# Optimization experiments

Measured on AMD Instinct MI355X. Metric: run time of the kernel, lower is better.

Reference implementation:

```python
import jax, jax.numpy as jnp
import numpy as np

B, S, VOCAB, D_MODEL, N_KERNELS, KSIZE, N_CLASSES = 8, 2048, 32000, 512, 256, 9, 4096
PAD = KSIZE // 2  # source uses kernel_size/2 (py2 int div)


def setup_inputs() -> dict:
    key = jax.random.key(0)
    ks = jax.random.split(key, 7)
    return {
        "text": jax.random.randint(ks[0], (B, S), 0, VOCAB),
        "embed_table": jax.random.normal(ks[1], (VOCAB, D_MODEL), dtype=jnp.float32) * 0.02,
        "conv_w": jax.random.normal(ks[2], (N_KERNELS, D_MODEL, KSIZE), dtype=jnp.float32) * 0.02,
        "conv_b": jax.random.normal(ks[3], (N_KERNELS,), dtype=jnp.float32) * 0.02,
        "U_w": jax.random.normal(ks[4], (N_CLASSES, N_KERNELS), dtype=jnp.float32) * 0.02,
        "final_w": jax.random.normal(ks[5], (N_CLASSES, N_KERNELS), dtype=jnp.float32) * 0.02,
        "final_b": jax.random.normal(ks[6], (N_CLASSES,), dtype=jnp.float32) * 0.02,
    }


def reference(text, embed_table, conv_w, conv_b, U_w, final_w, final_b):
    # Embedding lookup (tgt_embed); dropout is identity in eval mode.
    x = embed_table[text]                                  # [B, S, D]
    # Conv1d over sequence: NCH layout, OIH kernel, same-length padding.
    xc = jax.lax.conv_general_dilated(
        x.transpose(0, 2, 1), conv_w,
        window_strides=(1,), padding=[(PAD, PAD)],
        dimension_numbers=("NCH", "OIH", "NCH"))
    x = jnp.tanh(xc.transpose(0, 2, 1) + conv_b)           # [B, S, K]
    # Shared-query label attention: scores [B, n_classes, S].
    scores = jnp.einsum("ck,bsk->bcs", U_w, x)
    alpha = jax.nn.softmax(scores, axis=2)
    m = jnp.einsum("bcs,bsk->bck", alpha, x)               # [B, C, K]
    y = jnp.sum(final_w * m, axis=2) + final_b             # [B, C]
    return y
```

## Files before the change

### kernel.cpp

```cpp
#include <hip/hip_runtime.h>
#include <math.h>

#define B 8
#define S 2048
#define D_MODEL 512
#define NK 256
#define KSZ 9
#define NC 4096
#define PADW 4
#define SSPLIT 4
#define CM 64
#define CW (CM + 8)
#define NSTG (KSZ * 16)
#define NTILES ((S / SSPLIT) / 32)

typedef __attribute__((ext_vector_type(8))) short bf16x8;
typedef __attribute__((ext_vector_type(4))) float f32x4;

static __device__ __forceinline__ unsigned short f2bf(float f) {
    unsigned int u = __float_as_uint(f);
    unsigned int r = (u + 0x7fffu + ((u >> 16) & 1u)) >> 16;
    return (unsigned short)r;
}

#define GLOAD_LDS16(g, l) __builtin_amdgcn_global_load_lds( \
    (const __attribute__((address_space(1))) void*)(g),     \
    (__attribute__((address_space(3))) void*)(l), 16, 0, 0)

#define PREP_W (KSZ * NK * D_MODEL)
#define PREP_UF (NC * NK)
#define PREP_N (PREP_W + (2 * PREP_UF) / 4)
__global__ __launch_bounds__(256) void prep_all(
    const float* __restrict__ w, unsigned short* __restrict__ wtb,
    const float* __restrict__ U, unsigned short* __restrict__ Ub,
    const float* __restrict__ F, unsigned short* __restrict__ Fb)
{
    const float LOG2E = 1.44269504088896340736f;
    int idx = blockIdx.x * 256 + threadIdx.x;
    if (idx < PREP_W) {
        int dd  = idx & 31;
        int k   = (idx >> 5) & (NK - 1);
        int stg = idx >> 13;
        int t = stg >> 4, h = stg & 15;
        wtb[idx] = f2bf(w[((size_t)k * D_MODEL + h * 32 + dd) * KSZ + t]);
        return;
    }
    idx -= PREP_W;
    if (idx < PREP_UF / 4) {
        float4 v = ((const float4*)U)[idx];
        ushort4 o;
        o.x = f2bf(v.x * LOG2E); o.y = f2bf(v.y * LOG2E);
        o.z = f2bf(v.z * LOG2E); o.w = f2bf(v.w * LOG2E);
        ((ushort4*)Ub)[idx] = o;
        return;
    }
    idx -= PREP_UF / 4;
    if (idx < PREP_UF / 4) {
        float4 v = ((const float4*)F)[idx];
        ushort4 o;
        o.x = f2bf(v.x); o.y = f2bf(v.y);
        o.z = f2bf(v.z); o.w = f2bf(v.w);
        ((ushort4*)Fb)[idx] = o;
    }
}

__global__ __launch_bounds__(512, 2) void conv_mfma(
    const int* __restrict__ text, const float* __restrict__ emb,
    const unsigned short* __restrict__ wtb, const float* __restrict__ bias,
    unsigned short* __restrict__ xf)
{
    __shared__ unsigned short xs[CW * D_MODEL];
    const int b  = blockIdx.x >> 5;
    const int s0 = (blockIdx.x & 31) * CM;
    const int tid = threadIdx.x;

    for (int u = tid; u < CW * 64; u += 512) {
        int row = u >> 6, c = u & 63;
        int gs = s0 + row - PADW;
        float4 v0 = make_float4(0.f, 0.f, 0.f, 0.f), v1 = v0;
        if (gs >= 0 && gs < S) {
            int tok = text[b * S + gs];
            const float4* e4 = (const float4*)(emb + (size_t)tok * D_MODEL + c * 8);
            v0 = e4[0]; v1 = e4[1];
        }
        union { bf16x8 v; unsigned short us[8]; } pk;
        pk.us[0] = f2bf(v0.x); pk.us[1] = f2bf(v0.y);
        pk.us[2] = f2bf(v0.z); pk.us[3] = f2bf(v0.w);
        pk.us[4] = f2bf(v1.x); pk.us[5] = f2bf(v1.y);
        pk.us[6] = f2bf(v1.z); pk.us[7] = f2bf(v1.w);
        int phys = c ^ (row & 7);
        *(bf16x8*)(xs + row * D_MODEL + phys * 8) = pk.v;
    }
    __syncthreads();

    const int wv   = tid >> 6;
    const int lane = tid & 63;
    const int cl   = lane & 15;
    const int quad = lane >> 4;
    const int n0   = wv * 32;

    bf16x8 A0[4], A1[4], A2[4], B0[2], B1[2], B2[2];
    f32x4 acc[4][2] = {};

    #define LDB(BB, stg)                                                      \
        {                                                                     \
            const unsigned short* wp = wtb + (size_t)(stg) * (NK * 32)        \
                                       + (n0 + cl) * 32 + quad * 8;           \
            BB[0] = *(const bf16x8*)(wp);                                     \
            BB[1] = *(const bf16x8*)(wp + 16 * 32);                           \
        }
    #define LDA(AA, stg)                                                      \
        {                                                                     \
            int t_ = (stg) >> 4, h_ = (stg) & 15;                             \
            _Pragma("unroll")                                                 \
            for (int ms = 0; ms < 4; ms++) {                                  \
                int row = cl + ms * 16 + t_;                                  \
                int ph  = (h_ * 4 + quad) ^ (row & 7);                        \
                AA[ms] = *(const bf16x8*)(xs + row * D_MODEL + ph * 8);       \
            }                                                                 \
        }
    #define FENCE asm volatile("" ::: "memory");
    #define DOMFMA(AA, BB)                                                    \
        _Pragma("unroll")                                                     \
        for (int ms = 0; ms < 4; ms++) {                                      \
            acc[ms][0] = __builtin_amdgcn_mfma_f32_16x16x32_bf16(AA[ms], BB[0], acc[ms][0], 0, 0, 0); \
            acc[ms][1] = __builtin_amdgcn_mfma_f32_16x16x32_bf16(AA[ms], BB[1], acc[ms][1], 0, 0, 0); \
        }

    LDB(B0, 0) LDA(A0, 0) LDB(B1, 1) LDA(A1, 1) LDB(B2, 2) LDA(A2, 2) FENCE

    for (int ss = 0; ss < NSTG; ss += 3) {
        DOMFMA(A0, B0)
        if (ss + 3 < NSTG) { LDB(B0, ss + 3) LDA(A0, ss + 3) FENCE }
        DOMFMA(A1, B1)
        if (ss + 4 < NSTG) { LDB(B1, ss + 4) LDA(A1, ss + 4) FENCE }
        DOMFMA(A2, B2)
        if (ss + 5 < NSTG) { LDB(B2, ss + 5) LDA(A2, ss + 5) FENCE }
    }

    #pragma unroll
    for (int ns = 0; ns < 2; ns++) {
        const int k = n0 + ns * 16 + cl;
        const float bk = bias[k];
        #pragma unroll
        for (int ms = 0; ms < 4; ms++) {
            #pragma unroll
            for (int r = 0; r < 4; r++) {
                int s = s0 + ms * 16 + quad * 4 + r;
                float v = acc[ms][ns][r] + bk;
                float e = __expf(2.f * v);
                float th = 1.f - 2.f / (e + 1.f);
                xf[((size_t)b * S + s) * NK + k] = f2bf(th);
            }
        }
    }
}

#define WAITVM4 asm volatile("s_waitcnt vmcnt(4)" ::: "memory")
#define WAITVM0 asm volatile("s_waitcnt vmcnt(0)" ::: "memory")
__global__ __launch_bounds__(256, 3) void attn_mfma(
    const unsigned short* __restrict__ xf, const unsigned short* __restrict__ Ub,
    const unsigned short* __restrict__ Fb, float* __restrict__ pl,
    float* __restrict__ pg)
{
    __shared__ unsigned short xsa[3 * 32 * NK];
    const int b    = blockIdx.z;
    const int sp   = blockIdx.y;
    const int tid  = threadIdx.x;
    const int wv   = tid >> 6;
    const int lane = tid & 63;
    const int cl   = lane & 15;
    const int quad = lane >> 4;
    const int c0   = blockIdx.x * 64 + wv * 16;
    const int wvu  = __builtin_amdgcn_readfirstlane(wv);

    bf16x8 uf[8], ff[8];
    {
        const unsigned short* up = Ub + (size_t)(c0 + cl) * NK + quad * 8;
        const unsigned short* fp = Fb + (size_t)(c0 + cl) * NK + quad * 8;
        #pragma unroll
        for (int kk = 0; kk < 8; kk++) {
            uf[kk] = *(const bf16x8*)(up + kk * 32);
            ff[kk] = *(const bf16x8*)(fp + kk * 32);
        }
    }

    const int sbeg = sp * (S / SSPLIT);
    const unsigned short* xb = xf + ((size_t)b * S + sbeg) * NK;

    const unsigned short* ssrc[4];
    unsigned short* sdst[4];
    #pragma unroll
    for (int j = 0; j < 4; j++) {
        int C = j * 256 + tid;
        int r = C >> 5, p = C & 31;
        int jl = p ^ (r & 7);
        ssrc[j] = xb + (size_t)r * NK + jl * 8;
        sdst[j] = xsa + j * 2048 + wvu * 512;
    }

    #define STAGE(bb, t)                                                      \
        {                                                                     \
            _Pragma("unroll")                                                 \
            for (int j = 0; j < 4; j++)                                       \
                GLOAD_LDS16(ssrc[j] + (t) * (32 * NK), sdst[j] + (bb) * 8192);\
        }

    STAGE(0, 0)
    STAGE(1, 1)

    const int swz = cl & 7;
    const unsigned short* pE = xsa + cl * NK + (quad ^ swz) * 8;
    const unsigned short* pO = xsa + cl * NK + ((quad + 4) ^ swz) * 8;

    float l = 0.f, G = 0.f;

    #pragma unroll
    for (int t = 0; t < NTILES; t++) {
        if (t + 1 < NTILES) { WAITVM4; } else { WAITVM0; }
        __builtin_amdgcn_s_barrier();
        if (t + 2 < NTILES) STAGE((t + 2) % 3, t + 2)

        const int buf = t % 3;
        f32x4 sa[2] = {}, ga[2] = {};
        #pragma unroll
        for (int kk = 0; kk < 8; kk++) {
            const unsigned short* pp = (kk & 1) ? pO : pE;
            const int eo = buf * 8192 + (kk >> 1) * 64;
            bf16x8 a0 = *(const bf16x8*)(pp + eo);
            bf16x8 a1 = *(const bf16x8*)(pp + eo + 16 * NK);
            sa[0] = __builtin_amdgcn_mfma_f32_16x16x32_bf16(a0, uf[kk], sa[0], 0, 0, 0);
            ga[0] = __builtin_amdgcn_mfma_f32_16x16x32_bf16(a0, ff[kk], ga[0], 0, 0, 0);
            sa[1] = __builtin_amdgcn_mfma_f32_16x16x32_bf16(a1, uf[kk], sa[1], 0, 0, 0);
            ga[1] = __builtin_amdgcn_mfma_f32_16x16x32_bf16(a1, ff[kk], ga[1], 0, 0, 0);
        }

        #pragma unroll
        for (int r = 0; r < 4; r++) {
            float e0 = __builtin_amdgcn_exp2f(sa[0][r]);
            float e1 = __builtin_amdgcn_exp2f(sa[1][r]);
            l += e0 + e1;
            G += e0 * ga[0][r] + e1 * ga[1][r];
        }
    }

    l += __shfl_xor(l, 16); l += __shfl_xor(l, 32);
    G += __shfl_xor(G, 16); G += __shfl_xor(G, 32);
    if (lane < 16) {
        size_t idx = ((size_t)b * SSPLIT + sp) * NC + c0 + lane;
        pl[idx] = l; pg[idx] = G;
    }
}

__global__ __launch_bounds__(256) void combine_kernel(
    const float* __restrict__ pl, const float* __restrict__ pg,
    const float* __restrict__ fb, float* __restrict__ out)
{
    int idx = blockIdx.x * 256 + threadIdx.x;
    if (idx >= B * NC) return;
    int b = idx / NC, c = idx % NC;
    float l = 0.f, g = 0.f;
    #pragma unroll
    for (int sp = 0; sp < SSPLIT; sp++) {
        size_t i = ((size_t)b * SSPLIT + sp) * NC + c;
        l += pl[i];
        g += pg[i];
    }
    out[idx] = g / l + fb[c];
}

extern "C" void kernel_launch(void* const* d_in, const int* in_sizes, int n_in,
                              void* d_out, int out_size, void* d_ws, size_t ws_size,
                              hipStream_t stream) {
    const int*   text   = (const int*)  d_in[0];
    const float* emb    = (const float*)d_in[1];
    const float* conv_w = (const float*)d_in[2];
    const float* conv_b = (const float*)d_in[3];
    const float* U_w    = (const float*)d_in[4];
    const float* F_w    = (const float*)d_in[5];
    const float* f_b    = (const float*)d_in[6];
    float* out = (float*)d_out;

    char* ws = (char*)d_ws;
    unsigned short* xf  = (unsigned short*)ws; ws += (size_t)B * S * NK * 2;
    unsigned short* wtb = (unsigned short*)ws; ws += (size_t)KSZ * NK * D_MODEL * 2;
    unsigned short* Ub  = (unsigned short*)ws; ws += (size_t)NC * NK * 2;
    unsigned short* Fb  = (unsigned short*)ws; ws += (size_t)NC * NK * 2;
    float* pl = (float*)ws; ws += (size_t)SSPLIT * B * NC * 4;
    float* pg = (float*)ws; ws += (size_t)SSPLIT * B * NC * 4;

    prep_all<<<dim3((PREP_N + 255) / 256), 256, 0, stream>>>(conv_w, wtb, U_w, Ub, F_w, Fb);
    conv_mfma<<<dim3(B * S / CM), 512, 0, stream>>>(text, emb, wtb, conv_b, xf);
    attn_mfma<<<dim3(NC / 64, SSPLIT, B), 256, 0, stream>>>(xf, Ub, Fb, pl, pg);
    combine_kernel<<<dim3((B * NC + 255) / 256), 256, 0, stream>>>(pl, pg, f_b, out);
}
```

Measured before the change: 214.1 us.

## Switch attention kernel to 32x32x16 MFMA with 128 classes per block

Each wave in the attention kernel now covers 32 classes instead of 16 and uses 32x32x16 bf16 MFMA in place of pairs of 16x16x32 MFMAs. Grid blocks each handle 128 classes, which halves the number of blocks and the reloads of the x tiles from global memory and LDS per class. The cost is twice as many U/F fragment registers held per wave, and launch bounds drop from 3 to 2 blocks per CU, which reduces occupancy. The LDS swizzle addressing is recomputed to match the new fragment layout.

```diff
diff --git a/kernel.cpp b/kernel.cpp
--- a/kernel.cpp
+++ b/kernel.cpp
@@ -16,6 +16,7 @@
 
 typedef __attribute__((ext_vector_type(8))) short bf16x8;
 typedef __attribute__((ext_vector_type(4))) float f32x4;
+typedef __attribute__((ext_vector_type(16))) float f32x16;
 
 static __device__ __forceinline__ unsigned short f2bf(float f) {
     unsigned int u = __float_as_uint(f);
@@ -158,7 +159,7 @@
 
 #define WAITVM4 asm volatile("s_waitcnt vmcnt(4)" ::: "memory")
 #define WAITVM0 asm volatile("s_waitcnt vmcnt(0)" ::: "memory")
-__global__ __launch_bounds__(256, 3) void attn_mfma(
+__global__ __launch_bounds__(256, 2) void attn_mfma(
     const unsigned short* __restrict__ xf, const unsigned short* __restrict__ Ub,
     const unsigned short* __restrict__ Fb, float* __restrict__ pl,
     float* __restrict__ pg)
@@ -169,19 +170,19 @@
     const int tid  = threadIdx.x;
     const int wv   = tid >> 6;
     const int lane = tid & 63;
-    const int cl   = lane & 15;
-    const int quad = lane >> 4;
-    const int c0   = blockIdx.x * 64 + wv * 16;
+    const int row  = lane & 31;
+    const int bh   = lane >> 5;
+    const int c0   = blockIdx.x * 128 + wv * 32;
     const int wvu  = __builtin_amdgcn_readfirstlane(wv);
 
-    bf16x8 uf[8], ff[8];
+    bf16x8 uf[16], ff[16];
     {
-        const unsigned short* up = Ub + (size_t)(c0 + cl) * NK + quad * 8;
-        const unsigned short* fp = Fb + (size_t)(c0 + cl) * NK + quad * 8;
-        #pragma unroll
-        for (int kk = 0; kk < 8; kk++) {
-            uf[kk] = *(const bf16x8*)(up + kk * 32);
-            ff[kk] = *(const bf16x8*)(fp + kk * 32);
+        const unsigned short* up = Ub + (size_t)(c0 + row) * NK + bh * 8;
+        const unsigned short* fp = Fb + (size_t)(c0 + row) * NK + bh * 8;
+        #pragma unroll
+        for (int kk = 0; kk < 16; kk++) {
+            uf[kk] = *(const bf16x8*)(up + kk * 16);
+            ff[kk] = *(const bf16x8*)(fp + kk * 16);
         }
     }
 
@@ -209,10 +210,7 @@
     STAGE(0, 0)
     STAGE(1, 1)
 
-    const int swz = cl & 7;
-    const unsigned short* pE = xsa + cl * NK + (quad ^ swz) * 8;
-    const unsigned short* pO = xsa + cl * NK + ((quad + 4) ^ swz) * 8;
-
+    const int sw = row & 7;
     float l = 0.f, G = 0.f;
 
     #pragma unroll
@@ -221,32 +219,28 @@
         __builtin_amdgcn_s_barrier();
         if (t + 2 < NTILES) STAGE((t + 2) % 3, t + 2)
 
-        const int buf = t % 3;
-        f32x4 sa[2] = {}, ga[2] = {};
-        #pragma unroll
-        for (int kk = 0; kk < 8; kk++) {
-            const unsigned short* pp = (kk & 1) ? pO : pE;
-            const int eo = buf * 8192 + (kk >> 1) * 64;
-            bf16x8 a0 = *(const bf16x8*)(pp + eo);
-            bf16x8 a1 = *(const bf16x8*)(pp + eo + 16 * NK);
-            sa[0] = __builtin_amdgcn_mfma_f32_16x16x32_bf16(a0, uf[kk], sa[0], 0, 0, 0);
-            ga[0] = __builtin_amdgcn_mfma_f32_16x16x32_bf16(a0, ff[kk], ga[0], 0, 0, 0);
-            sa[1] = __builtin_amdgcn_mfma_f32_16x16x32_bf16(a1, uf[kk], sa[1], 0, 0, 0);
-            ga[1] = __builtin_amdgcn_mfma_f32_16x16x32_bf16(a1, ff[kk], ga[1], 0, 0, 0);
-        }
-
-        #pragma unroll
-        for (int r = 0; r < 4; r++) {
-            float e0 = __builtin_amdgcn_exp2f(sa[0][r]);
-            float e1 = __builtin_amdgcn_exp2f(sa[1][r]);
-            l += e0 + e1;
-            G += e0 * ga[0][r] + e1 * ga[1][r];
-        }
-    }
-
-    l += __shfl_xor(l, 16); l += __shfl_xor(l, 32);
-    G += __shfl_xor(G, 16); G += __shfl_xor(G, 32);
-    if (lane < 16) {
+        const unsigned short* bs = xsa + (t % 3) * 8192 + row * NK;
+        f32x16 sa = {}, ga = {};
+        #pragma unroll
+        for (int kk = 0; kk < 16; kk++) {
+            int ch = 2 * kk + bh;
+            int ph = (ch & ~7) | ((ch & 7) ^ sw);
+            bf16x8 a = *(const bf16x8*)(bs + ph * 8);
+            sa = __builtin_amdgcn_mfma_f32_32x32x16_bf16(a, uf[kk], sa, 0, 0, 0);
+            ga = __builtin_amdgcn_mfma_f32_32x32x16_bf16(a, ff[kk], ga, 0, 0, 0);
+        }
+
+        #pragma unroll
+        for (int r = 0; r < 16; r++) {
+            float e = __builtin_amdgcn_exp2f(sa[r]);
+            l += e;
+            G += e * ga[r];
+        }
+    }
+
+    l += __shfl_xor(l, 32);
+    G += __shfl_xor(G, 32);
+    if (lane < 32) {
         size_t idx = ((size_t)b * SSPLIT + sp) * NC + c0 + lane;
         pl[idx] = l; pg[idx] = G;
     }
@@ -291,6 +285,6 @@
 
     prep_all<<<dim3((PREP_N + 255) / 256), 256, 0, stream>>>(conv_w, wtb, U_w, Ub, F_w, Fb);
     conv_mfma<<<dim3(B * S / CM), 512, 0, stream>>>(text, emb, wtb, conv_b, xf);
-    attn_mfma<<<dim3(NC / 64, SSPLIT, B), 256, 0, stream>>>(xf, Ub, Fb, pl, pg);
+    attn_mfma<<<dim3(NC / 128, SSPLIT, B), 256, 0, stream>>>(xf, Ub, Fb, pl, pg);
     combine_kernel<<<dim3((B * NC + 255) / 256), 256, 0, stream>>>(pl, pg, f_b, out);
 }
```

Result: no change. 213.2 us (-0.4%).
